# Performance work log

Hardware: AMD Instinct MI355X
Metric: run time of the kernel (lower is better)

## Reference

```python
import jax, jax.numpy as jnp
import numpy as np

N = 8192   # nodes
D = 128    # uniform feature dim (arch = [128,128,128])
L = 2      # num_layers = len(arch)-1
EDGE_P = 0.01

def setup_inputs() -> dict:
    key = jax.random.key(0)
    ks = jax.random.split(key, 11)
    features = jax.random.normal(ks[0], (N, D), dtype=jnp.float32)
    # sparse symmetric adjacency with self-loops (diagonal forced True, as in forward)
    a = jax.random.uniform(ks[1], (N, N)) < EDGE_P
    mask = a | a.T | jnp.eye(N, dtype=bool)
    s = 1.0 / np.sqrt(D)
    def w(k):
        return (jax.random.normal(k, (L, D, D), dtype=jnp.float32) * s)
    def b(k):
        return jax.random.normal(k, (L, D), dtype=jnp.float32) * 0.01
    return {
        "features": features, "mask": mask,
        "Wq": w(ks[2]), "bq": b(ks[3]),
        "Wk": w(ks[4]), "bk": b(ks[5]),
        "Wv": w(ks[6]), "bv": b(ks[7]),
        "Wo": w(ks[8]), "bo": b(ks[9]),
    }

def reference(features, mask, Wq, bq, Wk, bk, Wv, bv, Wo, bo):
    h = features
    outputs = [h]
    for l in range(L):
        Q = h @ Wq[l] + bq[l]                      # [N, D]
        K = h @ Wk[l] + bk[l]
        V = h @ Wv[l] + bv[l]
        scores = (Q @ K.T) * (1.0 / jnp.sqrt(jnp.float32(K.shape[1])))  # [N, N]
        scores = jnp.where(mask, scores, -jnp.inf)
        attn = jax.nn.softmax(scores, axis=1)
        h = attn @ V                                # [N, D]
        h = h @ Wo[l] + bo[l]
        outputs.append(h)
    return tuple(outputs)
```

## Files before the change

kernel.cpp:

```cpp
#include <hip/hip_runtime.h>
#include <hip/hip_bf16.h>
#include <hip/hip_fp16.h>
#include <math.h>

#define N 8192
#define D 128
#define CAP 512

typedef _Float16 f16x2 __attribute__((ext_vector_type(2)));
typedef _Float16 f16x4 __attribute__((ext_vector_type(4)));
typedef _Float16 f16x8 __attribute__((ext_vector_type(8)));
typedef float    f32x4 __attribute__((ext_vector_type(4)));

__device__ __forceinline__ float dot2(f16x2 a, f16x2 b, float c) {
#if __has_builtin(__builtin_amdgcn_fdot2)
    return __builtin_amdgcn_fdot2(a, b, c, false);
#else
    return c + (float)a[0] * (float)b[0] + (float)a[1] * (float)b[1];
#endif
}

__device__ __forceinline__ float dot8(f16x8 a, f16x8 b) {
    float c0 = dot2(__builtin_shufflevector(a, a, 0, 1), __builtin_shufflevector(b, b, 0, 1), 0.f);
    float c1 = dot2(__builtin_shufflevector(a, a, 2, 3), __builtin_shufflevector(b, b, 2, 3), 0.f);
    c0 = dot2(__builtin_shufflevector(a, a, 4, 5), __builtin_shufflevector(b, b, 4, 5), c0);
    c1 = dot2(__builtin_shufflevector(a, a, 6, 7), __builtin_shufflevector(b, b, 6, 7), c1);
    return c0 + c1;
}

__global__ __launch_bounds__(256) void build_adj(const int* __restrict__ mask,
                                                 unsigned short* __restrict__ nbr,
                                                 int* __restrict__ deg) {
    const int i = blockIdx.x;
    __shared__ int cnt;
    if (threadIdx.x == 0) cnt = 0;
    __syncthreads();
    const int4* row = (const int4*)(mask + (size_t)i * N);
    for (int c = threadIdx.x; c < N / 4; c += 256) {
        int4 m4 = row[c];
        int base = 4 * c;
        if (m4.x) { int p = atomicAdd(&cnt, 1); if (p < CAP) nbr[(size_t)i * CAP + p] = (unsigned short)(base); }
        if (m4.y) { int p = atomicAdd(&cnt, 1); if (p < CAP) nbr[(size_t)i * CAP + p] = (unsigned short)(base + 1); }
        if (m4.z) { int p = atomicAdd(&cnt, 1); if (p < CAP) nbr[(size_t)i * CAP + p] = (unsigned short)(base + 2); }
        if (m4.w) { int p = atomicAdd(&cnt, 1); if (p < CAP) nbr[(size_t)i * CAP + p] = (unsigned short)(base + 3); }
    }
    __syncthreads();
    if (threadIdx.x == 0) deg[i] = (cnt > CAP) ? CAP : cnt;
}

__global__ __launch_bounds__(256) void qkv_gemm(const float* __restrict__ A,
                                                const float* __restrict__ Wq, const float* __restrict__ bq,
                                                const float* __restrict__ Wk, const float* __restrict__ bk,
                                                const float* __restrict__ Wv, const float* __restrict__ bv,
                                                __half* __restrict__ Qo, __half* __restrict__ Ko,
                                                __half* __restrict__ Vo,
                                                float* __restrict__ copy_out) {
    __shared__ float As[8][D];
    const int tid = threadIdx.x;
    const int r   = tid >> 5;
    const int jg  = tid & 31;
    const int i0  = blockIdx.x * 8;

    const float4 av = ((const float4*)(A + (size_t)i0 * D))[tid];
    ((float4*)&As[0][0])[tid] = av;
    ((float4*)(copy_out + (size_t)i0 * D))[tid] = av;
    __syncthreads();

    const float* Ws[3] = {Wq, Wk, Wv};
    const float* bs[3] = {bq, bk, bv};
    __half* Os[3] = {Qo, Ko, Vo};
    const size_t st[3] = {D, 2 * D, 2 * D};

    #pragma unroll
    for (int m = 0; m < 3; ++m) {
        float4 acc = *(const float4*)(bs[m] + 4 * jg);
        const float* W = Ws[m];
        #pragma unroll 8
        for (int k4 = 0; k4 < 32; ++k4) {
            const float4 a4 = *(const float4*)&As[r][4 * k4];
            const float* wb = W + (size_t)(4 * k4) * D + 4 * jg;
            const float4 w0 = *(const float4*)(wb);
            const float4 w1 = *(const float4*)(wb + D);
            const float4 w2 = *(const float4*)(wb + 2 * D);
            const float4 w3 = *(const float4*)(wb + 3 * D);
            acc.x += a4.x * w0.x + a4.y * w1.x + a4.z * w2.x + a4.w * w3.x;
            acc.y += a4.x * w0.y + a4.y * w1.y + a4.z * w2.y + a4.w * w3.y;
            acc.z += a4.x * w0.z + a4.y * w1.z + a4.z * w2.z + a4.w * w3.z;
            acc.w += a4.x * w0.w + a4.y * w1.w + a4.z * w2.w + a4.w * w3.w;
        }
        f16x4 h;
        h[0] = (_Float16)acc.x; h[1] = (_Float16)acc.y;
        h[2] = (_Float16)acc.z; h[3] = (_Float16)acc.w;
        *(f16x4*)(Os[m] + (size_t)(i0 + r) * st[m] + 4 * jg) = h;
    }
}

__global__ __launch_bounds__(256) void gemmO_qkv(const float* __restrict__ Aattn,
                                                 const float* __restrict__ Wo, const float* __restrict__ bo,
                                                 float* __restrict__ Hout,
                                                 const float* __restrict__ Wq, const float* __restrict__ bq,
                                                 const float* __restrict__ Wk, const float* __restrict__ bk,
                                                 const float* __restrict__ Wv, const float* __restrict__ bv,
                                                 __half* __restrict__ Qo, __half* __restrict__ Ko,
                                                 __half* __restrict__ Vo) {
    __shared__ float As[8][D];
    __shared__ float Hs[8][D];
    const int tid = threadIdx.x;
    const int r   = tid >> 5;
    const int jg  = tid & 31;
    const int i0  = blockIdx.x * 8;

    ((float4*)&As[0][0])[tid] = ((const float4*)(Aattn + (size_t)i0 * D))[tid];
    __syncthreads();

    {
        float4 acc = *(const float4*)(bo + 4 * jg);
        #pragma unroll 8
        for (int k4 = 0; k4 < 32; ++k4) {
            const float4 a4 = *(const float4*)&As[r][4 * k4];
            const float* wb = Wo + (size_t)(4 * k4) * D + 4 * jg;
            const float4 w0 = *(const float4*)(wb);
            const float4 w1 = *(const float4*)(wb + D);
            const float4 w2 = *(const float4*)(wb + 2 * D);
            const float4 w3 = *(const float4*)(wb + 3 * D);
            acc.x += a4.x * w0.x + a4.y * w1.x + a4.z * w2.x + a4.w * w3.x;
            acc.y += a4.x * w0.y + a4.y * w1.y + a4.z * w2.y + a4.w * w3.y;
            acc.z += a4.x * w0.z + a4.y * w1.z + a4.z * w2.z + a4.w * w3.z;
            acc.w += a4.x * w0.w + a4.y * w1.w + a4.z * w2.w + a4.w * w3.w;
        }
        *(float4*)(Hout + (size_t)(i0 + r) * D + 4 * jg) = acc;
        *(float4*)&Hs[r][4 * jg] = acc;
    }
    __syncthreads();

    const float* Ws[3] = {Wq, Wk, Wv};
    const float* bs[3] = {bq, bk, bv};
    __half* Os[3] = {Qo, Ko, Vo};
    const size_t st[3] = {D, 2 * D, 2 * D};
    #pragma unroll
    for (int m = 0; m < 3; ++m) {
        float4 acc = *(const float4*)(bs[m] + 4 * jg);
        const float* W = Ws[m];
        #pragma unroll 8
        for (int k4 = 0; k4 < 32; ++k4) {
            const float4 a4 = *(const float4*)&Hs[r][4 * k4];
            const float* wb = W + (size_t)(4 * k4) * D + 4 * jg;
            const float4 w0 = *(const float4*)(wb);
            const float4 w1 = *(const float4*)(wb + D);
            const float4 w2 = *(const float4*)(wb + 2 * D);
            const float4 w3 = *(const float4*)(wb + 3 * D);
            acc.x += a4.x * w0.x + a4.y * w1.x + a4.z * w2.x + a4.w * w3.x;
            acc.y += a4.x * w0.y + a4.y * w1.y + a4.z * w2.y + a4.w * w3.y;
            acc.z += a4.x * w0.z + a4.y * w1.z + a4.z * w2.z + a4.w * w3.z;
            acc.w += a4.x * w0.w + a4.y * w1.w + a4.z * w2.w + a4.w * w3.w;
        }
        f16x4 h;
        h[0] = (_Float16)acc.x; h[1] = (_Float16)acc.y;
        h[2] = (_Float16)acc.z; h[3] = (_Float16)acc.w;
        *(f16x4*)(Os[m] + (size_t)(i0 + r) * st[m] + 4 * jg) = h;
    }
}

__global__ __launch_bounds__(256) void gemm_bias(const float* __restrict__ A,
                                                 const float* __restrict__ W,
                                                 const float* __restrict__ bias,
                                                 float* __restrict__ C) {
    __shared__ float As[8][D];
    const int tid = threadIdx.x;
    const int r   = tid >> 5;
    const int jg  = tid & 31;
    const int i0  = blockIdx.x * 8;

    ((float4*)&As[0][0])[tid] = ((const float4*)(A + (size_t)i0 * D))[tid];
    __syncthreads();

    float4 acc = *(const float4*)(bias + 4 * jg);
    #pragma unroll 8
    for (int k4 = 0; k4 < 32; ++k4) {
        const float4 a4 = *(const float4*)&As[r][4 * k4];
        const float* wb = W + (size_t)(4 * k4) * D + 4 * jg;
        const float4 w0 = *(const float4*)(wb);
        const float4 w1 = *(const float4*)(wb + D);
        const float4 w2 = *(const float4*)(wb + 2 * D);
        const float4 w3 = *(const float4*)(wb + 3 * D);
        acc.x += a4.x * w0.x + a4.y * w1.x + a4.z * w2.x + a4.w * w3.x;
        acc.y += a4.x * w0.y + a4.y * w1.y + a4.z * w2.y + a4.w * w3.y;
        acc.z += a4.x * w0.z + a4.y * w1.z + a4.z * w2.z + a4.w * w3.z;
        acc.w += a4.x * w0.w + a4.y * w1.w + a4.z * w2.w + a4.w * w3.w;
    }
    *(float4*)(C + (size_t)(i0 + r) * D + 4 * jg) = acc;
}

__global__ __launch_bounds__(256) void attn_sparse(const __half* __restrict__ Q,
                                                   const __half* __restrict__ KV,
                                                   const unsigned short* __restrict__ nbr,
                                                   const int* __restrict__ deg,
                                                   float* __restrict__ Hout) {
    const int tid  = threadIdx.x;
    const int wave = tid >> 6;
    const int lane = tid & 63;
    const int g    = lane >> 4;
    const int gl   = lane & 15;
    const int i    = blockIdx.x * 4 + wave;

    __shared__ unsigned short jls[4][CAP];

    const int dg = min(deg[i], CAP);
    for (int e = lane; e < dg; e += 64)
        jls[wave][e] = __builtin_nontemporal_load(&nbr[(size_t)i * CAP + e]);
    const f16x8 qv = ((const f16x8*)(Q + (size_t)i * D))[gl];
    __syncthreads();

    const float scale = 0.088388347648318447f;

    float acc[8] = {0.f, 0.f, 0.f, 0.f, 0.f, 0.f, 0.f, 0.f};
    float denom  = 0.f;

    int e = g;
    int jc = (e < dg) ? (int)jls[wave][e] : 0;
    const f16x8* kvp = (const f16x8*)(KV + (size_t)jc * (2 * D));
    f16x8 kc = kvp[gl];
    f16x8 vc = kvp[16 + gl];

    while (e < dg) {
        const int en = e + 4;
        const int jn = (en < dg) ? (int)jls[wave][en] : 0;
        const f16x8* kvpn = (const f16x8*)(KV + (size_t)jn * (2 * D));
        const f16x8 kn = kvpn[gl];
        const f16x8 vn = kvpn[16 + gl];

        float dot = dot8(kc, qv);
        dot += __shfl_xor(dot, 1);
        dot += __shfl_xor(dot, 2);
        dot += __shfl_xor(dot, 4);
        dot += __shfl_xor(dot, 8);
        const float p = __expf(dot * scale);
        #pragma unroll
        for (int k = 0; k < 8; ++k) acc[k] += p * (float)vc[k];
        denom += p;

        e = en; kc = kn; vc = vn;
    }

    #pragma unroll
    for (int k = 0; k < 8; ++k) {
        acc[k] += __shfl_xor(acc[k], 16);
        acc[k] += __shfl_xor(acc[k], 32);
    }
    denom += __shfl_xor(denom, 16);
    denom += __shfl_xor(denom, 32);

    if (g == 0) {
        const float inv = 1.0f / denom;
        f32x4 o0, o1;
        o0[0] = acc[0] * inv; o0[1] = acc[1] * inv; o0[2] = acc[2] * inv; o0[3] = acc[3] * inv;
        o1[0] = acc[4] * inv; o1[1] = acc[5] * inv; o1[2] = acc[6] * inv; o1[3] = acc[7] * inv;
        f32x4* dst = (f32x4*)(Hout + (size_t)i * D + 8 * gl);
        __builtin_nontemporal_store(o0, &dst[0]);
        __builtin_nontemporal_store(o1, &dst[1]);
    }
}

extern "C" void kernel_launch(void* const* d_in, const int* in_sizes, int n_in,
                              void* d_out, int out_size, void* d_ws, size_t ws_size,
                              hipStream_t stream) {
    const float* features = (const float*)d_in[0];
    const int*   mask     = (const int*)d_in[1];
    const float* Wq = (const float*)d_in[2];
    const float* bq = (const float*)d_in[3];
    const float* Wk = (const float*)d_in[4];
    const float* bk = (const float*)d_in[5];
    const float* Wv = (const float*)d_in[6];
    const float* bv = (const float*)d_in[7];
    const float* Wo = (const float*)d_in[8];
    const float* bo = (const float*)d_in[9];
    float* out = (float*)d_out;

    char* base = (char*)d_ws;
    unsigned short* nbr = (unsigned short*)base;
    int*    deg  = (int*)(base + (size_t)N * CAP * 2);
    __half* Qb16 = (__half*)(base + (size_t)N * CAP * 2 + N * 4);
    __half* KVb  = Qb16 + (size_t)N * D;
    float*  tmp  = (float*)(KVb + (size_t)N * 2 * D);

    build_adj<<<N, 256, 0, stream>>>(mask, nbr, deg);

    qkv_gemm<<<N / 8, 256, 0, stream>>>(features, Wq, bq, Wk, bk, Wv, bv,
                                        Qb16, KVb, KVb + D, out);
    attn_sparse<<<N / 4, 256, 0, stream>>>(Qb16, KVb, nbr, deg, tmp);
    gemmO_qkv<<<N / 8, 256, 0, stream>>>(tmp, Wo, bo, out + (size_t)N * D,
                                         Wq + D * D, bq + D, Wk + D * D, bk + D,
                                         Wv + D * D, bv + D, Qb16, KVb, KVb + D);
    attn_sparse<<<N / 4, 256, 0, stream>>>(Qb16, KVb, nbr, deg, tmp);
    gemm_bias<<<N / 8, 256, 0, stream>>>(tmp, Wo + D * D, bo + D,
                                         out + (size_t)2 * N * D);
}
```

Before: 574.7 us.

## Fuse adjacency build with first QKV GEMM and simplify attention loop

Merges the adjacency-list construction and the first-layer QKV projection into one launch, with blocks split by index range, so the two independent tasks share a grid and one launch is removed. In the sparse attention kernel, the manual software prefetch of the next neighbor's K/V is dropped in favor of a plain loop, and launch bounds request 8 blocks per CU. Together these aim for higher occupancy and fewer launches. The cost is that each load's latency is no longer hidden by prefetch and is left to wave-level parallelism instead.

```diff
diff --git a/kernel.cpp b/kernel.cpp
--- a/kernel.cpp
+++ b/kernel.cpp
@@ -28,38 +28,41 @@
     return c0 + c1;
 }
 
-__global__ __launch_bounds__(256) void build_adj(const int* __restrict__ mask,
-                                                 unsigned short* __restrict__ nbr,
-                                                 int* __restrict__ deg) {
-    const int i = blockIdx.x;
-    __shared__ int cnt;
-    if (threadIdx.x == 0) cnt = 0;
-    __syncthreads();
-    const int4* row = (const int4*)(mask + (size_t)i * N);
-    for (int c = threadIdx.x; c < N / 4; c += 256) {
-        int4 m4 = row[c];
-        int base = 4 * c;
-        if (m4.x) { int p = atomicAdd(&cnt, 1); if (p < CAP) nbr[(size_t)i * CAP + p] = (unsigned short)(base); }
-        if (m4.y) { int p = atomicAdd(&cnt, 1); if (p < CAP) nbr[(size_t)i * CAP + p] = (unsigned short)(base + 1); }
-        if (m4.z) { int p = atomicAdd(&cnt, 1); if (p < CAP) nbr[(size_t)i * CAP + p] = (unsigned short)(base + 2); }
-        if (m4.w) { int p = atomicAdd(&cnt, 1); if (p < CAP) nbr[(size_t)i * CAP + p] = (unsigned short)(base + 3); }
-    }
-    __syncthreads();
-    if (threadIdx.x == 0) deg[i] = (cnt > CAP) ? CAP : cnt;
-}
-
-__global__ __launch_bounds__(256) void qkv_gemm(const float* __restrict__ A,
-                                                const float* __restrict__ Wq, const float* __restrict__ bq,
-                                                const float* __restrict__ Wk, const float* __restrict__ bk,
-                                                const float* __restrict__ Wv, const float* __restrict__ bv,
-                                                __half* __restrict__ Qo, __half* __restrict__ Ko,
-                                                __half* __restrict__ Vo,
-                                                float* __restrict__ copy_out) {
+__global__ __launch_bounds__(256) void adj_qkv(const int* __restrict__ mask,
+                                               unsigned short* __restrict__ nbr,
+                                               int* __restrict__ deg,
+                                               const float* __restrict__ A,
+                                               const float* __restrict__ Wq, const float* __restrict__ bq,
+                                               const float* __restrict__ Wk, const float* __restrict__ bk,
+                                               const float* __restrict__ Wv, const float* __restrict__ bv,
+                                               __half* __restrict__ Qo, __half* __restrict__ Ko,
+                                               __half* __restrict__ Vo,
+                                               float* __restrict__ copy_out) {
     __shared__ float As[8][D];
     const int tid = threadIdx.x;
+
+    if (blockIdx.x < N) {
+        const int i = blockIdx.x;
+        __shared__ int cnt;
+        if (tid == 0) cnt = 0;
+        __syncthreads();
+        const int4* row = (const int4*)(mask + (size_t)i * N);
+        for (int c = tid; c < N / 4; c += 256) {
+            int4 m4 = row[c];
+            int base = 4 * c;
+            if (m4.x) { int p = atomicAdd(&cnt, 1); if (p < CAP) nbr[(size_t)i * CAP + p] = (unsigned short)(base); }
+            if (m4.y) { int p = atomicAdd(&cnt, 1); if (p < CAP) nbr[(size_t)i * CAP + p] = (unsigned short)(base + 1); }
+            if (m4.z) { int p = atomicAdd(&cnt, 1); if (p < CAP) nbr[(size_t)i * CAP + p] = (unsigned short)(base + 2); }
+            if (m4.w) { int p = atomicAdd(&cnt, 1); if (p < CAP) nbr[(size_t)i * CAP + p] = (unsigned short)(base + 3); }
+        }
+        __syncthreads();
+        if (tid == 0) deg[i] = (cnt > CAP) ? CAP : cnt;
+        return;
+    }
+
     const int r   = tid >> 5;
     const int jg  = tid & 31;
-    const int i0  = blockIdx.x * 8;
+    const int i0  = (blockIdx.x - N) * 8;
 
     const float4 av = ((const float4*)(A + (size_t)i0 * D))[tid];
     ((float4*)&As[0][0])[tid] = av;
@@ -191,11 +194,11 @@
     *(float4*)(C + (size_t)(i0 + r) * D + 4 * jg) = acc;
 }
 
-__global__ __launch_bounds__(256) void attn_sparse(const __half* __restrict__ Q,
-                                                   const __half* __restrict__ KV,
-                                                   const unsigned short* __restrict__ nbr,
-                                                   const int* __restrict__ deg,
-                                                   float* __restrict__ Hout) {
+__global__ __launch_bounds__(256, 8) void attn_sparse(const __half* __restrict__ Q,
+                                                      const __half* __restrict__ KV,
+                                                      const unsigned short* __restrict__ nbr,
+                                                      const int* __restrict__ deg,
+                                                      float* __restrict__ Hout) {
     const int tid  = threadIdx.x;
     const int wave = tid >> 6;
     const int lane = tid & 63;
@@ -216,30 +219,20 @@
     float acc[8] = {0.f, 0.f, 0.f, 0.f, 0.f, 0.f, 0.f, 0.f};
     float denom  = 0.f;
 
-    int e = g;
-    int jc = (e < dg) ? (int)jls[wave][e] : 0;
-    const f16x8* kvp = (const f16x8*)(KV + (size_t)jc * (2 * D));
-    f16x8 kc = kvp[gl];
-    f16x8 vc = kvp[16 + gl];
-
-    while (e < dg) {
-        const int en = e + 4;
-        const int jn = (en < dg) ? (int)jls[wave][en] : 0;
-        const f16x8* kvpn = (const f16x8*)(KV + (size_t)jn * (2 * D));
-        const f16x8 kn = kvpn[gl];
-        const f16x8 vn = kvpn[16 + gl];
-
-        float dot = dot8(kc, qv);
+    for (int e = g; e < dg; e += 4) {
+        const int j = jls[wave][e];
+        const f16x8* kvp = (const f16x8*)(KV + (size_t)j * (2 * D));
+        const f16x8 kv = kvp[gl];
+        const f16x8 v8 = kvp[16 + gl];
+        float dot = dot8(kv, qv);
         dot += __shfl_xor(dot, 1);
         dot += __shfl_xor(dot, 2);
         dot += __shfl_xor(dot, 4);
         dot += __shfl_xor(dot, 8);
         const float p = __expf(dot * scale);
         #pragma unroll
-        for (int k = 0; k < 8; ++k) acc[k] += p * (float)vc[k];
+        for (int k = 0; k < 8; ++k) acc[k] += p * (float)v8[k];
         denom += p;
-
-        e = en; kc = kn; vc = vn;
     }
 
     #pragma unroll
@@ -283,10 +276,9 @@
     __half* KVb  = Qb16 + (size_t)N * D;
     float*  tmp  = (float*)(KVb + (size_t)N * 2 * D);
 
-    build_adj<<<N, 256, 0, stream>>>(mask, nbr, deg);
-
-    qkv_gemm<<<N / 8, 256, 0, stream>>>(features, Wq, bq, Wk, bk, Wv, bv,
-                                        Qb16, KVb, KVb + D, out);
+    adj_qkv<<<N + N / 8, 256, 0, stream>>>(mask, nbr, deg,
+                                           features, Wq, bq, Wk, bk, Wv, bv,
+                                           Qb16, KVb, KVb + D, out);
     attn_sparse<<<N / 4, 256, 0, stream>>>(Qb16, KVb, nbr, deg, tmp);
     gemmO_qkv<<<N / 8, 256, 0, stream>>>(tmp, Wo, bo, out + (size_t)N * D,
                                          Wq + D * D, bq + D, Wk + D * D, bk + D,
```

Measured after the change: 569.3 us. Within noise of the previous version (-0.9%).
